# Kernel tuning notes

Hardware: AMD Instinct MI355X
Metric: run time of the kernel (lower is better)

## Reference

```python
import jax, jax.numpy as jnp
import numpy as np

FEAT_DIM = 128
TIME_DIM = 128
D_MODEL = FEAT_DIM + TIME_DIM  # 256
N_HEAD = 2
D_K = D_MODEL // N_HEAD  # 128
B, N = 4096, 64


def setup_inputs() -> dict:
    key = jax.random.key(0)
    ks = jax.random.split(key, 16)
    s = lambda k, sh, sc=0.05: jax.random.normal(k, sh, dtype=jnp.float32) * sc
    return {
        "src": jax.random.normal(ks[0], (B, FEAT_DIM), dtype=jnp.float32),
        "src_t": jax.random.normal(ks[1], (B, 1, TIME_DIM), dtype=jnp.float32),
        "seq": jax.random.normal(ks[2], (B, N, FEAT_DIM), dtype=jnp.float32),
        "seq_t": jax.random.normal(ks[3], (B, N, TIME_DIM), dtype=jnp.float32),
        "mask": jax.random.randint(ks[4], (B, N), 0, 2).astype(jnp.bool_),
        # attention params (x @ W convention, W: [d_model, n_head*d_k])
        "w_qs": s(ks[5], (D_MODEL, N_HEAD * D_K)),
        "w_ks": s(ks[6], (D_MODEL, N_HEAD * D_K)),
        "w_vs": s(ks[7], (D_MODEL, N_HEAD * D_K)),
        "fc_w": s(ks[8], (N_HEAD * D_K, D_MODEL)),
        "fc_b": jnp.zeros((D_MODEL,), jnp.float32),
        "ln_g": jnp.ones((D_MODEL,), jnp.float32),
        "ln_b": jnp.zeros((D_MODEL,), jnp.float32),
        # MergeLayer params: fc1 [(d_model+feat), feat], fc2 [feat, feat]
        "fc1_w": s(ks[9], (D_MODEL + FEAT_DIM, FEAT_DIM)),
        "fc1_b": jnp.zeros((FEAT_DIM,), jnp.float32),
        "fc2_w": s(ks[10], (FEAT_DIM, FEAT_DIM)),
        "fc2_b": jnp.zeros((FEAT_DIM,), jnp.float32),
    }


def _layer_norm(x, g, b, eps=1e-5):
    mu = jnp.mean(x, axis=-1, keepdims=True)
    var = jnp.mean((x - mu) ** 2, axis=-1, keepdims=True)
    return (x - mu) * jax.lax.rsqrt(var + eps) * g + b


def reference(src, src_t, seq, seq_t, mask,
              w_qs, w_ks, w_vs, fc_w, fc_b, ln_g, ln_b,
              fc1_w, fc1_b, fc2_w, fc2_b):
    # q: [B,1,D_MODEL] = cat(src, src_t); k=v: [B,N,D_MODEL]
    q_in = jnp.concatenate([src[:, None, :], src_t], axis=2)
    k_in = jnp.concatenate([seq, seq_t], axis=2)

    q = (q_in @ w_qs).reshape(B, 1, N_HEAD, D_K)   # [B,1,H,dk]
    k = (k_in @ w_ks).reshape(B, N, N_HEAD, D_K)   # [B,N,H,dk]
    v = (k_in @ w_vs).reshape(B, N, N_HEAD, D_K)   # [B,N,H,dv]

    # scaled dot-product attention, len_q == 1
    attn = jnp.einsum('bqhd,bkhd->bhqk', q, k) / jnp.sqrt(jnp.float32(D_K))
    attn = jnp.where(mask[:, None, None, :], jnp.float32(-1e10), attn)
    attn = jax.nn.softmax(attn, axis=-1)           # [B,H,1,N]

    out = jnp.einsum('bhqk,bkhd->bqhd', attn, v).reshape(B, 1, N_HEAD * D_K)
    out = out @ fc_w + fc_b                         # dropout is identity (eval)
    out = _layer_norm(out + q_in, ln_g, ln_b)       # [B,1,D_MODEL]

    out = out[:, 0, :]                              # squeeze -> [B,D_MODEL]
    # MergeLayer: cat(out, src) -> fc1 -> relu -> fc2
    h = jnp.concatenate([out, src], axis=1)
    h = jax.nn.relu(h @ fc1_w + fc1_b)
    merged = h @ fc2_w + fc2_b                      # [B, FEAT_DIM]

    # attn squeeze: [n_head*B, N] ordering matches torch view(n_head, B, ...)
    attn_sq = jnp.transpose(attn[:, :, 0, :], (1, 0, 2)).reshape(N_HEAD * B, N)
    return merged, attn_sq
```

## Files before the change

### kernel.cpp

```cpp
#include <hip/hip_runtime.h>


__device__ __forceinline__ void fma4(float4& a, float s, const float4& w) {
  a.x = fmaf(s, w.x, a.x); a.y = fmaf(s, w.y, a.y);
  a.z = fmaf(s, w.z, a.z); a.w = fmaf(s, w.w, a.w);
}
__device__ __forceinline__ float dot4(const float4& a, const float4& b) {
  return a.x * b.x + a.y * b.y + a.z * b.z + a.w * b.w;
}

__global__ __launch_bounds__(256) void k_wf(const float* __restrict__ w_qs,
                                            const float* __restrict__ w_ks,
                                            float* __restrict__ W) {
  const int idx = blockIdx.x * 256 + threadIdx.x;
  const int c = idx >> 9;
  const int col = idx & 511;
  const int h = col >> 8;
  const int j = col & 255;
  const float* a = w_qs + c * 256 + h * 128;
  const float* bk = w_ks + j * 256 + h * 128;
  float acc = 0.f;
#pragma unroll
  for (int d = 0; d < 128; d += 4)
    acc += dot4(*(const float4*)&a[d], *(const float4*)&bk[d]);
  W[idx] = acc * 0.08838834764831845f;
}

__global__ __launch_bounds__(256) void k_qk(const float* __restrict__ src,
                                            const float* __restrict__ srct,
                                            const float* __restrict__ W,
                                            float* __restrict__ QK) {
  __shared__ float sQ[16 * 256];
  const int tid = threadIdx.x;
  const int rb = (blockIdx.x >> 1) * 16;
  const int ch = (blockIdx.x & 1) * 256;
  {
    const int r = tid >> 4;
    const int cb = (tid & 15) * 16;
#pragma unroll
    for (int i = 0; i < 4; ++i) {
      const int c = cb + i * 4;
      float4 v = (c < 128) ? *(const float4*)&src[(rb + r) * 128 + c]
                           : *(const float4*)&srct[(rb + r) * 128 + (c - 128)];
      *(float4*)&sQ[r * 256 + c] = v;
    }
  }
  __syncthreads();
  const int rg = tid >> 6;
  const int cg = tid & 63;
  const int col = ch + cg * 4;
  float4 acc[4] = {};
  for (int k = 0; k < 256; k += 4) {
    const float4 w0 = *(const float4*)&W[(k + 0) * 512 + col];
    const float4 w1 = *(const float4*)&W[(k + 1) * 512 + col];
    const float4 w2 = *(const float4*)&W[(k + 2) * 512 + col];
    const float4 w3 = *(const float4*)&W[(k + 3) * 512 + col];
#pragma unroll
    for (int r = 0; r < 4; ++r) {
      const float4 a = *(const float4*)&sQ[(rg * 4 + r) * 256 + k];
      fma4(acc[r], a.x, w0); fma4(acc[r], a.y, w1);
      fma4(acc[r], a.z, w2); fma4(acc[r], a.w, w3);
    }
  }
#pragma unroll
  for (int r = 0; r < 4; ++r)
    *(float4*)&QK[(rb + rg * 4 + r) * 512 + col] = acc[r];
}

__global__ __launch_bounds__(256) void k_attn(const float* __restrict__ seq,
                                              const float* __restrict__ seqt,
                                              const unsigned int* __restrict__ mw,
                                              float* QKS,
                                              float* __restrict__ att) {
  __shared__ float sqk[4][512];
  __shared__ float se0[4][64];
  __shared__ float se1[4][64];
  __shared__ int nlist[4][64];
  const int tid = threadIdx.x;
  const int lane = tid & 63;
  const int w = tid >> 6;
  const int b0 = blockIdx.x * 4;
  const int b = b0 + w;
#pragma unroll
  for (int i = 0; i < 2; ++i) {
    const int f4 = i * 256 + tid;
    const int g = f4 >> 7;
    const int c = (f4 & 127) * 4;
    *(float4*)&sqk[g][c] = *(const float4*)&QKS[(b0 + g) * 512 + c];
  }
  __syncthreads();

  const bool masked = (mw[b * 64 + lane] != 0u);
  const float* srow = seq + b * 8192 + lane * 128;
  const float* trow = seqt + b * 8192 + lane * 128;
  float p0s = 0.f, p0t = 0.f, p1s = 0.f, p1t = 0.f;
  if (!masked) {
#pragma unroll 4
    for (int i = 0; i < 32; ++i) {
      const float4 ks = *(const float4*)&srow[i * 4];
      const float4 kt = *(const float4*)&trow[i * 4];
      const float4 q0s = *(const float4*)&sqk[w][i * 4];
      const float4 q0t = *(const float4*)&sqk[w][128 + i * 4];
      const float4 q1s = *(const float4*)&sqk[w][256 + i * 4];
      const float4 q1t = *(const float4*)&sqk[w][384 + i * 4];
      p0s += dot4(ks, q0s); p0t += dot4(kt, q0t);
      p1s += dot4(ks, q1s); p1t += dot4(kt, q1t);
    }
  }
  const float e0 = masked ? 0.f : __expf(p0s + p0t);
  const float e1 = masked ? 0.f : __expf(p1s + p1t);
  float l0 = e0, l1 = e1;
#pragma unroll
  for (int off = 32; off >= 1; off >>= 1) {
    l0 += __shfl_xor(l0, off);
    l1 += __shfl_xor(l1, off);
  }
  const float a0 = e0 / l0;
  const float a1 = e1 / l1;
  att[b * 64 + lane] = a0;
  att[4096 * 64 + b * 64 + lane] = a1;

  const unsigned long long bits = __ballot(!masked);
  const int cnt = __popcll(bits);
  const int pos = __popcll(bits & ((1ull << lane) - 1ull));
  if (!masked) nlist[w][pos] = lane;
  se0[w][lane] = a0;
  se1[w][lane] = a1;
  __syncthreads();

  const float* kin = (lane < 32) ? (seq + b * 8192 + lane * 4)
                                 : (seqt + b * 8192 + (lane - 32) * 4);
  float4 s0 = {0.f, 0.f, 0.f, 0.f}, s1 = {0.f, 0.f, 0.f, 0.f};
  int t = 0;
  for (; t + 4 <= cnt; t += 4) {
    const int n0 = nlist[w][t + 0];
    const int n1 = nlist[w][t + 1];
    const int n2 = nlist[w][t + 2];
    const int n3 = nlist[w][t + 3];
    const float4 k0 = *(const float4*)(kin + n0 * 128);
    const float4 k1 = *(const float4*)(kin + n1 * 128);
    const float4 k2 = *(const float4*)(kin + n2 * 128);
    const float4 k3 = *(const float4*)(kin + n3 * 128);
    fma4(s0, se0[w][n0], k0); fma4(s1, se1[w][n0], k0);
    fma4(s0, se0[w][n1], k1); fma4(s1, se1[w][n1], k1);
    fma4(s0, se0[w][n2], k2); fma4(s1, se1[w][n2], k2);
    fma4(s0, se0[w][n3], k3); fma4(s1, se1[w][n3], k3);
  }
  for (; t < cnt; ++t) {
    const int n = nlist[w][t];
    const float4 kv = *(const float4*)(kin + n * 128);
    fma4(s0, se0[w][n], kv);
    fma4(s1, se1[w][n], kv);
  }
  *(float4*)(QKS + b * 512 + lane * 4) = s0;
  *(float4*)(QKS + b * 512 + 256 + lane * 4) = s1;
}

__global__ __launch_bounds__(256) void k_epi(
    const float* __restrict__ S, const float* __restrict__ src,
    const float* __restrict__ srct, const float* __restrict__ w_vs,
    const float* __restrict__ fc_w, const float* __restrict__ fc_b,
    const float* __restrict__ ln_g, const float* __restrict__ ln_b,
    const float* __restrict__ fc1_w, const float* __restrict__ fc1_b,
    const float* __restrict__ fc2_w, const float* __restrict__ fc2_b,
    float* __restrict__ out) {
  __shared__ float sv[4][512];
  __shared__ float qin[4][256];
  __shared__ float ov[4][256];
  __shared__ float xx[4][256];
  __shared__ float hcat[4][384];
  __shared__ float h1[4][128];
  __shared__ float stats[4][2];
  const int tid = threadIdx.x;
  const int b0 = blockIdx.x * 4;

#pragma unroll
  for (int i = 0; i < 2; ++i) {
    const int f4 = i * 256 + tid;
    const int g = f4 >> 7;
    const int c = (f4 & 127) * 4;
    *(float4*)&sv[g][c] = *(const float4*)&S[(b0 + g) * 512 + c];
  }
  {
    const int g = tid >> 6;
    const int c = (tid & 63) * 4;
    float4 v = (c < 128) ? *(const float4*)&src[(b0 + g) * 128 + c]
                         : *(const float4*)&srct[(b0 + g) * 128 + (c - 128)];
    *(float4*)&qin[g][c] = v;
  }
  __syncthreads();

  {
    const int h = tid >> 7;
    float acc[4] = {0.f, 0.f, 0.f, 0.f};
    for (int t = 0; t < 256; ++t) {
      const float w = w_vs[t * 256 + tid];
#pragma unroll
      for (int g = 0; g < 4; ++g) acc[g] = fmaf(sv[g][h * 256 + t], w, acc[g]);
    }
#pragma unroll
    for (int g = 0; g < 4; ++g) ov[g][tid] = acc[g];
  }
  __syncthreads();

  {
    float acc[4] = {0.f, 0.f, 0.f, 0.f};
    for (int d = 0; d < 256; ++d) {
      const float w = fc_w[d * 256 + tid];
#pragma unroll
      for (int g = 0; g < 4; ++g) acc[g] = fmaf(ov[g][d], w, acc[g]);
    }
    const float fb = fc_b[tid];
#pragma unroll
    for (int g = 0; g < 4; ++g) xx[g][tid] = acc[g] + fb + qin[g][tid];
  }
  __syncthreads();

  if (tid < 4) {
    const int g = tid;
    float s = 0.f, ss = 0.f;
    for (int j = 0; j < 256; ++j) {
      const float x = xx[g][j];
      s += x; ss += x * x;
    }
    const float mu = s * (1.0f / 256.0f);
    const float var = ss * (1.0f / 256.0f) - mu * mu;
    stats[g][0] = mu;
    stats[g][1] = rsqrtf(var + 1e-5f);
  }
  __syncthreads();
  {
    const float gg = ln_g[tid], bb = ln_b[tid];
#pragma unroll
    for (int g = 0; g < 4; ++g)
      hcat[g][tid] = (xx[g][tid] - stats[g][0]) * stats[g][1] * gg + bb;
  }
#pragma unroll
  for (int i = 0; i < 2; ++i) {
    const int idx = i * 256 + tid;
    const int g = idx >> 7, c = idx & 127;
    hcat[g][256 + c] = src[(b0 + g) * 128 + c];
  }
  __syncthreads();

  {
    const int col = tid & 127;
    const int gp = (tid >> 7) * 2;
    float acc0 = fc1_b[col], acc1 = acc0;
    for (int d = 0; d < 384; ++d) {
      const float w = fc1_w[d * 128 + col];
      acc0 = fmaf(hcat[gp][d], w, acc0);
      acc1 = fmaf(hcat[gp + 1][d], w, acc1);
    }
    h1[gp][col] = fmaxf(acc0, 0.f);
    h1[gp + 1][col] = fmaxf(acc1, 0.f);
  }
  __syncthreads();

  {
    const int col = tid & 127;
    const int gp = (tid >> 7) * 2;
    float acc0 = fc2_b[col], acc1 = acc0;
    for (int d = 0; d < 128; ++d) {
      const float w = fc2_w[d * 128 + col];
      acc0 = fmaf(h1[gp][d], w, acc0);
      acc1 = fmaf(h1[gp + 1][d], w, acc1);
    }
    out[(b0 + gp) * 128 + col] = acc0;
    out[(b0 + gp + 1) * 128 + col] = acc1;
  }
}

extern "C" void kernel_launch(void* const* d_in, const int* in_sizes, int n_in,
                              void* d_out, int out_size, void* d_ws,
                              size_t ws_size, hipStream_t stream) {
  (void)in_sizes; (void)n_in; (void)out_size; (void)ws_size;
  const float* src = (const float*)d_in[0];
  const float* srct = (const float*)d_in[1];
  const float* seq = (const float*)d_in[2];
  const float* seqt = (const float*)d_in[3];
  const unsigned int* mask = (const unsigned int*)d_in[4];
  const float* w_qs = (const float*)d_in[5];
  const float* w_ks = (const float*)d_in[6];
  const float* w_vs = (const float*)d_in[7];
  const float* fc_w = (const float*)d_in[8];
  const float* fc_b = (const float*)d_in[9];
  const float* ln_g = (const float*)d_in[10];
  const float* ln_b = (const float*)d_in[11];
  const float* fc1_w = (const float*)d_in[12];
  const float* fc1_b = (const float*)d_in[13];
  const float* fc2_w = (const float*)d_in[14];
  const float* fc2_b = (const float*)d_in[15];
  float* out = (float*)d_out;
  float* att = out + 4096 * 128;
  float* W = (float*)d_ws;
  float* QKS = W + 256 * 512;
  k_wf<<<512, 256, 0, stream>>>(w_qs, w_ks, W);
  k_qk<<<512, 256, 0, stream>>>(src, srct, W, QKS);
  k_attn<<<1024, 256, 0, stream>>>(seq, seqt, mask, QKS, att);
  k_epi<<<1024, 256, 0, stream>>>(QKS, src, srct, w_vs, fc_w, fc_b, ln_g,
                                  ln_b, fc1_w, fc1_b, fc2_w, fc2_b, out);
}
```

Measured before the change: 432.9 us.

## Split attention per batch across four waves and parallelize epilogue LayerNorm

The attention kernel now gives each block a single batch row, with four waves each covering a 64-wide slice of the key feature dimension. Partial dot products are combined through shared memory, and the weighted sum is done per scalar column. This raises parallelism and memory-level concurrency on the dominant seq/seq_t reads, at the cost of extra barriers and narrower loads. The epilogue also replaces the four-thread serial LayerNorm reduction with wave shuffles, unrolls its GEMV loops by four using float4 shared-memory reads, and reuses qin instead of re-reading src.

```diff
diff --git a/kernel.cpp b/kernel.cpp
--- a/kernel.cpp
+++ b/kernel.cpp
@@ -72,43 +72,45 @@
                                               const unsigned int* __restrict__ mw,
                                               float* QKS,
                                               float* __restrict__ att) {
-  __shared__ float sqk[4][512];
-  __shared__ float se0[4][64];
-  __shared__ float se1[4][64];
-  __shared__ int nlist[4][64];
+  __shared__ float sqk[512];
+  __shared__ float part0[4][64];
+  __shared__ float part1[4][64];
+  __shared__ float sa0[64];
+  __shared__ float sa1[64];
+  __shared__ int nlist[64];
   const int tid = threadIdx.x;
   const int lane = tid & 63;
   const int w = tid >> 6;
-  const int b0 = blockIdx.x * 4;
-  const int b = b0 + w;
-#pragma unroll
-  for (int i = 0; i < 2; ++i) {
-    const int f4 = i * 256 + tid;
-    const int g = f4 >> 7;
-    const int c = (f4 & 127) * 4;
-    *(float4*)&sqk[g][c] = *(const float4*)&QKS[(b0 + g) * 512 + c];
-  }
-  __syncthreads();
-
+  const int b = blockIdx.x;
+
+  if (tid < 128)
+    *(float4*)&sqk[tid * 4] = *(const float4*)&QKS[b * 512 + tid * 4];
   const bool masked = (mw[b * 64 + lane] != 0u);
-  const float* srow = seq + b * 8192 + lane * 128;
-  const float* trow = seqt + b * 8192 + lane * 128;
-  float p0s = 0.f, p0t = 0.f, p1s = 0.f, p1t = 0.f;
+  __syncthreads();
+
+  const float* rowp = (w < 2) ? (seq + b * 8192 + lane * 128 + w * 64)
+                              : (seqt + b * 8192 + lane * 128 + (w - 2) * 64);
+  float p0 = 0.f, p1 = 0.f;
   if (!masked) {
-#pragma unroll 4
-    for (int i = 0; i < 32; ++i) {
-      const float4 ks = *(const float4*)&srow[i * 4];
-      const float4 kt = *(const float4*)&trow[i * 4];
-      const float4 q0s = *(const float4*)&sqk[w][i * 4];
-      const float4 q0t = *(const float4*)&sqk[w][128 + i * 4];
-      const float4 q1s = *(const float4*)&sqk[w][256 + i * 4];
-      const float4 q1t = *(const float4*)&sqk[w][384 + i * 4];
-      p0s += dot4(ks, q0s); p0t += dot4(kt, q0t);
-      p1s += dot4(ks, q1s); p1t += dot4(kt, q1t);
-    }
-  }
-  const float e0 = masked ? 0.f : __expf(p0s + p0t);
-  const float e1 = masked ? 0.f : __expf(p1s + p1t);
+    const float* q0 = &sqk[w * 64];
+    const float* q1 = &sqk[256 + w * 64];
+#pragma unroll 8
+    for (int i = 0; i < 16; ++i) {
+      const float4 kv = *(const float4*)&rowp[i * 4];
+      p0 += dot4(kv, *(const float4*)&q0[i * 4]);
+      p1 += dot4(kv, *(const float4*)&q1[i * 4]);
+    }
+  }
+  part0[w][lane] = p0;
+  part1[w][lane] = p1;
+  __syncthreads();
+
+  const float fp0 =
+      part0[0][lane] + part0[1][lane] + part0[2][lane] + part0[3][lane];
+  const float fp1 =
+      part1[0][lane] + part1[1][lane] + part1[2][lane] + part1[3][lane];
+  const float e0 = masked ? 0.f : __expf(fp0);
+  const float e1 = masked ? 0.f : __expf(fp1);
   float l0 = e0, l1 = e1;
 #pragma unroll
   for (int off = 32; off >= 1; off >>= 1) {
@@ -117,43 +119,44 @@
   }
   const float a0 = e0 / l0;
   const float a1 = e1 / l1;
-  att[b * 64 + lane] = a0;
-  att[4096 * 64 + b * 64 + lane] = a1;
-
   const unsigned long long bits = __ballot(!masked);
+  if (w == 0) {
+    att[b * 64 + lane] = a0;
+    att[4096 * 64 + b * 64 + lane] = a1;
+    sa0[lane] = a0;
+    sa1[lane] = a1;
+    const int pos = __popcll(bits & ((1ull << lane) - 1ull));
+    if (!masked) nlist[pos] = lane;
+  }
+  __syncthreads();
+
   const int cnt = __popcll(bits);
-  const int pos = __popcll(bits & ((1ull << lane) - 1ull));
-  if (!masked) nlist[w][pos] = lane;
-  se0[w][lane] = a0;
-  se1[w][lane] = a1;
-  __syncthreads();
-
-  const float* kin = (lane < 32) ? (seq + b * 8192 + lane * 4)
-                                 : (seqt + b * 8192 + (lane - 32) * 4);
-  float4 s0 = {0.f, 0.f, 0.f, 0.f}, s1 = {0.f, 0.f, 0.f, 0.f};
+  const float* kin2 = (w < 2) ? (seq + b * 8192 + w * 64 + lane)
+                              : (seqt + b * 8192 + (w - 2) * 64 + lane);
+  float s0 = 0.f, s1 = 0.f;
   int t = 0;
   for (; t + 4 <= cnt; t += 4) {
-    const int n0 = nlist[w][t + 0];
-    const int n1 = nlist[w][t + 1];
-    const int n2 = nlist[w][t + 2];
-    const int n3 = nlist[w][t + 3];
-    const float4 k0 = *(const float4*)(kin + n0 * 128);
-    const float4 k1 = *(const float4*)(kin + n1 * 128);
-    const float4 k2 = *(const float4*)(kin + n2 * 128);
-    const float4 k3 = *(const float4*)(kin + n3 * 128);
-    fma4(s0, se0[w][n0], k0); fma4(s1, se1[w][n0], k0);
-    fma4(s0, se0[w][n1], k1); fma4(s1, se1[w][n1], k1);
-    fma4(s0, se0[w][n2], k2); fma4(s1, se1[w][n2], k2);
-    fma4(s0, se0[w][n3], k3); fma4(s1, se1[w][n3], k3);
+    const int n0 = nlist[t + 0];
+    const int n1 = nlist[t + 1];
+    const int n2 = nlist[t + 2];
+    const int n3 = nlist[t + 3];
+    const float k0 = kin2[n0 * 128];
+    const float k1 = kin2[n1 * 128];
+    const float k2 = kin2[n2 * 128];
+    const float k3 = kin2[n3 * 128];
+    s0 = fmaf(sa0[n0], k0, s0); s1 = fmaf(sa1[n0], k0, s1);
+    s0 = fmaf(sa0[n1], k1, s0); s1 = fmaf(sa1[n1], k1, s1);
+    s0 = fmaf(sa0[n2], k2, s0); s1 = fmaf(sa1[n2], k2, s1);
+    s0 = fmaf(sa0[n3], k3, s0); s1 = fmaf(sa1[n3], k3, s1);
   }
   for (; t < cnt; ++t) {
-    const int n = nlist[w][t];
-    const float4 kv = *(const float4*)(kin + n * 128);
-    fma4(s0, se0[w][n], kv);
-    fma4(s1, se1[w][n], kv);
-  }
-  *(float4*)(QKS + b * 512 + lane * 4) = s0;
-  *(float4*)(QKS + b * 512 + 256 + lane * 4) = s1;
+    const int n = nlist[t];
+    const float kv = kin2[n * 128];
+    s0 = fmaf(sa0[n], kv, s0);
+    s1 = fmaf(sa1[n], kv, s1);
+  }
+  QKS[b * 512 + w * 64 + lane] = s0;
+  QKS[b * 512 + 256 + w * 64 + lane] = s1;
 }
 
 __global__ __launch_bounds__(256) void k_epi(
@@ -167,11 +170,12 @@
   __shared__ float sv[4][512];
   __shared__ float qin[4][256];
   __shared__ float ov[4][256];
-  __shared__ float xx[4][256];
   __shared__ float hcat[4][384];
   __shared__ float h1[4][128];
-  __shared__ float stats[4][2];
+  __shared__ float red[4][4][2];
   const int tid = threadIdx.x;
+  const int lane = tid & 63;
+  const int wv = tid >> 6;
   const int b0 = blockIdx.x * 4;
 
 #pragma unroll
@@ -190,56 +194,81 @@
   }
   __syncthreads();
 
-  {
-    const int h = tid >> 7;
+  const int h = tid >> 7;
+  {
     float acc[4] = {0.f, 0.f, 0.f, 0.f};
-    for (int t = 0; t < 256; ++t) {
-      const float w = w_vs[t * 256 + tid];
-#pragma unroll
-      for (int g = 0; g < 4; ++g) acc[g] = fmaf(sv[g][h * 256 + t], w, acc[g]);
+    for (int t = 0; t < 256; t += 4) {
+      const float w0 = w_vs[(t + 0) * 256 + tid];
+      const float w1 = w_vs[(t + 1) * 256 + tid];
+      const float w2 = w_vs[(t + 2) * 256 + tid];
+      const float w3 = w_vs[(t + 3) * 256 + tid];
+#pragma unroll
+      for (int g = 0; g < 4; ++g) {
+        const float4 s4 = *(const float4*)&sv[g][h * 256 + t];
+        acc[g] = fmaf(s4.x, w0, acc[g]);
+        acc[g] = fmaf(s4.y, w1, acc[g]);
+        acc[g] = fmaf(s4.z, w2, acc[g]);
+        acc[g] = fmaf(s4.w, w3, acc[g]);
+      }
     }
 #pragma unroll
     for (int g = 0; g < 4; ++g) ov[g][tid] = acc[g];
   }
   __syncthreads();
 
+  float x[4];
   {
     float acc[4] = {0.f, 0.f, 0.f, 0.f};
-    for (int d = 0; d < 256; ++d) {
-      const float w = fc_w[d * 256 + tid];
-#pragma unroll
-      for (int g = 0; g < 4; ++g) acc[g] = fmaf(ov[g][d], w, acc[g]);
+    for (int d = 0; d < 256; d += 4) {
+      const float w0 = fc_w[(d + 0) * 256 + tid];
+      const float w1 = fc_w[(d + 1) * 256 + tid];
+      const float w2 = fc_w[(d + 2) * 256 + tid];
+      const float w3 = fc_w[(d + 3) * 256 + tid];
+#pragma unroll
+      for (int g = 0; g < 4; ++g) {
+        const float4 o4 = *(const float4*)&ov[g][d];
+        acc[g] = fmaf(o4.x, w0, acc[g]);
+        acc[g] = fmaf(o4.y, w1, acc[g]);
+        acc[g] = fmaf(o4.z, w2, acc[g]);
+        acc[g] = fmaf(o4.w, w3, acc[g]);
+      }
     }
     const float fb = fc_b[tid];
 #pragma unroll
-    for (int g = 0; g < 4; ++g) xx[g][tid] = acc[g] + fb + qin[g][tid];
-  }
-  __syncthreads();
-
-  if (tid < 4) {
-    const int g = tid;
-    float s = 0.f, ss = 0.f;
-    for (int j = 0; j < 256; ++j) {
-      const float x = xx[g][j];
-      s += x; ss += x * x;
-    }
-    const float mu = s * (1.0f / 256.0f);
-    const float var = ss * (1.0f / 256.0f) - mu * mu;
-    stats[g][0] = mu;
-    stats[g][1] = rsqrtf(var + 1e-5f);
+    for (int g = 0; g < 4; ++g) x[g] = acc[g] + fb + qin[g][tid];
+  }
+
+#pragma unroll
+  for (int g = 0; g < 4; ++g) {
+    float s = x[g];
+    float q = x[g] * x[g];
+#pragma unroll
+    for (int off = 32; off >= 1; off >>= 1) {
+      s += __shfl_xor(s, off);
+      q += __shfl_xor(q, off);
+    }
+    if (lane == 0) {
+      red[wv][g][0] = s;
+      red[wv][g][1] = q;
+    }
   }
   __syncthreads();
   {
     const float gg = ln_g[tid], bb = ln_b[tid];
 #pragma unroll
-    for (int g = 0; g < 4; ++g)
-      hcat[g][tid] = (xx[g][tid] - stats[g][0]) * stats[g][1] * gg + bb;
+    for (int g = 0; g < 4; ++g) {
+      const float s = red[0][g][0] + red[1][g][0] + red[2][g][0] + red[3][g][0];
+      const float q = red[0][g][1] + red[1][g][1] + red[2][g][1] + red[3][g][1];
+      const float mu = s * (1.0f / 256.0f);
+      const float rstd = rsqrtf(q * (1.0f / 256.0f) - mu * mu + 1e-5f);
+      hcat[g][tid] = (x[g] - mu) * rstd * gg + bb;
+    }
   }
 #pragma unroll
   for (int i = 0; i < 2; ++i) {
     const int idx = i * 256 + tid;
     const int g = idx >> 7, c = idx & 127;
-    hcat[g][256 + c] = src[(b0 + g) * 128 + c];
+    hcat[g][256 + c] = qin[g][c];
   }
   __syncthreads();
 
@@ -247,10 +276,17 @@
     const int col = tid & 127;
     const int gp = (tid >> 7) * 2;
     float acc0 = fc1_b[col], acc1 = acc0;
-    for (int d = 0; d < 384; ++d) {
-      const float w = fc1_w[d * 128 + col];
-      acc0 = fmaf(hcat[gp][d], w, acc0);
-      acc1 = fmaf(hcat[gp + 1][d], w, acc1);
+    for (int d = 0; d < 384; d += 4) {
+      const float w0 = fc1_w[(d + 0) * 128 + col];
+      const float w1 = fc1_w[(d + 1) * 128 + col];
+      const float w2 = fc1_w[(d + 2) * 128 + col];
+      const float w3 = fc1_w[(d + 3) * 128 + col];
+      const float4 a4 = *(const float4*)&hcat[gp][d];
+      const float4 b4 = *(const float4*)&hcat[gp + 1][d];
+      acc0 = fmaf(a4.x, w0, acc0); acc0 = fmaf(a4.y, w1, acc0);
+      acc0 = fmaf(a4.z, w2, acc0); acc0 = fmaf(a4.w, w3, acc0);
+      acc1 = fmaf(b4.x, w0, acc1); acc1 = fmaf(b4.y, w1, acc1);
+      acc1 = fmaf(b4.z, w2, acc1); acc1 = fmaf(b4.w, w3, acc1);
     }
     h1[gp][col] = fmaxf(acc0, 0.f);
     h1[gp + 1][col] = fmaxf(acc1, 0.f);
@@ -261,10 +297,17 @@
     const int col = tid & 127;
     const int gp = (tid >> 7) * 2;
     float acc0 = fc2_b[col], acc1 = acc0;
-    for (int d = 0; d < 128; ++d) {
-      const float w = fc2_w[d * 128 + col];
-      acc0 = fmaf(h1[gp][d], w, acc0);
-      acc1 = fmaf(h1[gp + 1][d], w, acc1);
+    for (int d = 0; d < 128; d += 4) {
+      const float w0 = fc2_w[(d + 0) * 128 + col];
+      const float w1 = fc2_w[(d + 1) * 128 + col];
+      const float w2 = fc2_w[(d + 2) * 128 + col];
+      const float w3 = fc2_w[(d + 3) * 128 + col];
+      const float4 a4 = *(const float4*)&h1[gp][d];
+      const float4 b4 = *(const float4*)&h1[gp + 1][d];
+      acc0 = fmaf(a4.x, w0, acc0); acc0 = fmaf(a4.y, w1, acc0);
+      acc0 = fmaf(a4.z, w2, acc0); acc0 = fmaf(a4.w, w3, acc0);
+      acc1 = fmaf(b4.x, w0, acc1); acc1 = fmaf(b4.y, w1, acc1);
+      acc1 = fmaf(b4.z, w2, acc1); acc1 = fmaf(b4.w, w3, acc1);
     }
     out[(b0 + gp) * 128 + col] = acc0;
     out[(b0 + gp + 1) * 128 + col] = acc1;
@@ -297,7 +340,7 @@
   float* QKS = W + 256 * 512;
   k_wf<<<512, 256, 0, stream>>>(w_qs, w_ks, W);
   k_qk<<<512, 256, 0, stream>>>(src, srct, W, QKS);
-  k_attn<<<1024, 256, 0, stream>>>(seq, seqt, mask, QKS, att);
+  k_attn<<<4096, 256, 0, stream>>>(seq, seqt, mask, QKS, att);
   k_epi<<<1024, 256, 0, stream>>>(QKS, src, srct, w_vs, fc_w, fc_b, ln_g,
                                   ln_b, fc1_w, fc1_b, fc2_w, fc2_b, out);
 }
```

Result: faster. 384.5 us (-11.2%).
